# Optimization experiments

Measured on AMD Instinct MI355X. Metric: run time of the kernel, lower is better.

Reference implementation:

```python
import jax, jax.numpy as jnp
import numpy as np
import math

N_NODES = 50000
N_EDGES = 800000
IN_DIM = 128
HID = 128
OUT_DIM = 2048
N_LABEL_EDGES = 4096
POOL_RATIO = 0.5
NUM_HEADS = 8


def seg_sum(x, idx, n):
    return jax.ops.segment_sum(x, idx, num_segments=n)


def graph_conv(x, W, b, src, dst, emask, n):
    # DGL GraphConv, norm='both': D_out^-1/2 A D_in^-1/2 (x W) + b (masked edges)
    deg_out = seg_sum(emask, src, n)
    deg_in = seg_sum(emask, dst, n)
    ns = jax.lax.rsqrt(jnp.maximum(deg_out, 1.0))
    nd = jax.lax.rsqrt(jnp.maximum(deg_in, 1.0))
    h = x @ W
    msg = (h * ns[:, None])[src] * emask[:, None]
    agg = seg_sum(msg, dst, n)
    return agg * nd[:, None] + b


def conv_pool_block(x, src, dst, emask, cW, cb, sW, sb):
    # GraphConv -> ReLU -> SAGPool(top-k by GraphConv score, tanh gate) -> avg||max readout
    n = x.shape[0]
    h = jax.nn.relu(graph_conv(x, cW, cb, src, dst, emask, n))
    score = graph_conv(h, sW, sb, src, dst, emask, n)[:, 0]
    k = int(math.ceil(POOL_RATIO * n))  # static
    _, perm = jax.lax.top_k(score, k)
    h_new = h[perm] * jnp.tanh(score[perm])[:, None]
    # remap edges to the pooled node set; drop edges touching removed nodes via mask
    newid = jnp.full((n,), -1, jnp.int32).at[perm].set(jnp.arange(k, dtype=jnp.int32))
    nsrc = newid[src]
    ndst = newid[dst]
    new_mask = emask * (nsrc >= 0).astype(emask.dtype) * (ndst >= 0).astype(emask.dtype)
    nsrc = jnp.maximum(nsrc, 0)
    ndst = jnp.maximum(ndst, 0)
    readout = jnp.concatenate([h_new.mean(0), h_new.max(0)])[None, :]  # [1, 2*HID]
    return h_new, nsrc, ndst, new_mask, readout


def gat_conv(x, fcW, al, ar, lsrc, ldst, n, slope=0.2):
    # GATConv(1 -> 1, num_heads=8): head feature dim is 1
    h = x @ fcW                      # [n, heads]
    el = h * al
    er = h * ar
    e = jax.nn.leaky_relu(el[lsrc] + er[ldst], slope)  # [E_l, heads]
    emax = jax.ops.segment_max(e, ldst, num_segments=n)
    emax = jnp.where(jnp.isfinite(emax), emax, 0.0)
    ex = jnp.exp(e - emax[ldst])
    denom = seg_sum(ex, ldst, n)
    alpha = ex / jnp.maximum(denom[ldst], 1e-9)
    out = seg_sum(alpha * h[lsrc], ldst, n)            # [n, heads]
    return out[:, :, None]                             # [n, heads, 1]


def setup_inputs() -> dict:
    key = jax.random.key(0)
    ks = jax.random.split(key, 32)

    def rn(k, shape, s=0.05):
        return jax.random.normal(k, shape, jnp.float32) * s

    inp = {}
    inp['feat'] = jax.random.normal(ks[0], (N_NODES, IN_DIM), jnp.float32)
    inp['sequence_feature'] = jax.random.normal(ks[1], (1, 1024), jnp.float32)
    inp['src'] = jax.random.randint(ks[2], (N_EDGES,), 0, N_NODES, jnp.int32)
    inp['dst'] = jax.random.randint(ks[3], (N_EDGES,), 0, N_NODES, jnp.int32)
    inp['label_src'] = jax.random.randint(ks[4], (N_LABEL_EDGES,), 0, OUT_DIM, jnp.int32)
    inp['label_dst'] = jax.random.randint(ks[5], (N_LABEL_EDGES,), 0, OUT_DIM, jnp.int32)
    i = 6
    for b in range(3):
        din = IN_DIM if b == 0 else HID
        inp['cW%d' % b] = rn(ks[i], (din, HID)); i += 1
        inp['cb%d' % b] = jnp.zeros((HID,), jnp.float32)
        inp['sW%d' % b] = rn(ks[i], (HID, 1)); i += 1
        inp['sb%d' % b] = jnp.zeros((1,), jnp.float32)
    inp['lin1W'] = rn(ks[i], (2 * HID + 1024, 2 * HID)); i += 1
    inp['lin1b'] = jnp.zeros((2 * HID,), jnp.float32)
    inp['lin2W'] = rn(ks[i], (2 * HID, HID)); i += 1
    inp['lin2b'] = jnp.zeros((HID,), jnp.float32)
    inp['lin3W'] = rn(ks[i], (HID, OUT_DIM)); i += 1
    inp['lin3b'] = jnp.zeros((OUT_DIM,), jnp.float32)
    inp['gat_fcW'] = rn(ks[i], (1, NUM_HEADS)); i += 1
    inp['gat_al'] = rn(ks[i], (NUM_HEADS,)); i += 1
    inp['gat_ar'] = rn(ks[i], (NUM_HEADS,)); i += 1
    return inp


def reference(feat, sequence_feature, src, dst, label_src, label_dst,
              cW0, cb0, sW0, sb0, cW1, cb1, sW1, sb1, cW2, cb2, sW2, sb2,
              lin1W, lin1b, lin2W, lin2b, lin3W, lin3b,
              gat_fcW, gat_al, gat_ar):
    x, s, d = feat, src, dst
    emask = jnp.ones((src.shape[0],), jnp.float32)
    final = None
    for cW, cb, sW, sb in ((cW0, cb0, sW0, sb0), (cW1, cb1, sW1, sb1), (cW2, cb2, sW2, sb2)):
        x, s, d, emask, ro = conv_pool_block(x, s, d, emask, cW, cb, sW, sb)
        final = ro if final is None else final + ro
    final = jnp.concatenate([final, sequence_feature], axis=-1)  # [1, 2*HID+1024]
    f = jax.nn.relu(final @ lin1W + lin1b)
    # dropout: eval mode -> identity
    f = jax.nn.relu(f @ lin2W + lin2b)
    f = f @ lin3W + lin3b          # [1, OUT_DIM]
    ft = f.T                       # [OUT_DIM, 1]
    gat_out = gat_conv(ft, gat_fcW, gat_al, gat_ar, label_src, label_dst, OUT_DIM)
    max_value = jnp.max(gat_out, axis=1)      # [OUT_DIM, 1]
    _ = ft - jax.nn.relu(max_value)           # computed then discarded, as in source
    return ft.T
```

## Files before the change

kernel.cpp:

```cpp
#include <hip/hip_runtime.h>
#include <hip/hip_bf16.h>
#include <cmath>

#define N0 50000
#define NEDGE 800000
#define NEG_HUGE -3.402823466e38f
#define STRIDE 128
#define HBINS 12500
#define HSLICE 16

typedef int i32x4 __attribute__((ext_vector_type(4)));
typedef __attribute__((ext_vector_type(8))) short short8v;
typedef __attribute__((ext_vector_type(4))) float f32x4;

__device__ inline float b2f(unsigned short u) { return __uint_as_float(((unsigned)u) << 16); }

__device__ inline unsigned short f2b(float f) {
    __hip_bfloat16 h = __float2bfloat16(f);
    return *(unsigned short*)&h;
}

__device__ inline unsigned fkey(float f) {
    unsigned b = __float_as_uint(f);
    if (b == 0x80000000u) b = 0u;
    return (b & 0x80000000u) ? ~b : (b | 0x80000000u);
}

__device__ inline void atomicMaxF(float* a, float v) {
    if (v >= 0.f) atomicMax((int*)a, __float_as_int(v));
    else          atomicMin((unsigned int*)a, __float_as_uint(v));
}

__global__ void k_init(float* finalv, float* f1raw, int* deg_out, int* fill,
                       int* binsA, int* binsB, float* maxbuf, int* ctrl) {
    int i = blockIdx.x * blockDim.x + threadIdx.x;
    if (i < 256) { finalv[i] = 0.f; f1raw[i] = 0.f; }
    if (i < 384) maxbuf[i] = NEG_HUGE;
    if (i < N0) { deg_out[i] = 0; fill[i] = 0; }
    if (i < 65536) { binsA[i] = 0; binsB[i] = 0; }
    if (i < 2) ctrl[8 + i] = 0;
}

__global__ __launch_bounds__(1024) void k_hist(const int* __restrict__ esrc,
                                               unsigned* __restrict__ deg_part) {
    __shared__ unsigned hist[HBINS];
    int b = blockIdx.x;
    int r = b & 3;
    int slice = b >> 2;
    for (int i = threadIdx.x; i < HBINS; i += 1024) hist[i] = 0;
    __syncthreads();
    int lo = r * HBINS;
    int base = slice * (NEDGE / HSLICE);
    for (int e = threadIdx.x * 4; e < NEDGE / HSLICE; e += 4096) {
        i32x4 a = __builtin_nontemporal_load((const i32x4*)(esrc + base + e));
        int ss[4] = {a.x, a.y, a.z, a.w};
#pragma unroll
        for (int q = 0; q < 4; ++q) {
            unsigned loc = (unsigned)(ss[q] - lo);
            if (loc < (unsigned)HBINS) atomicAdd(&hist[loc], 1u);
        }
    }
    __syncthreads();
    for (int i = threadIdx.x; i < HBINS; i += 1024)
        deg_part[(size_t)slice * N0 + lo + i] = hist[i];
}

__global__ void k_dsum(const unsigned* __restrict__ deg_part, int* deg_out) {
    int v = blockIdx.x * 256 + threadIdx.x;
    if (v >= N0) return;
    unsigned s = 0;
#pragma unroll
    for (int q = 0; q < HSLICE; ++q) s += deg_part[(size_t)q * N0 + v];
    deg_out[v] = (int)s;
}

__global__ __launch_bounds__(256) void k_build(
        const int* __restrict__ esrc, const int* __restrict__ edst,
        int* fill, int* csr_src) {
    int t = blockIdx.x * 256 + threadIdx.x;
    int e0 = t * 4;
    if (e0 >= NEDGE) return;
    i32x4 a = __builtin_nontemporal_load((const i32x4*)(esrc + e0));
    i32x4 bq = __builtin_nontemporal_load((const i32x4*)(edst + e0));
    int s[4] = {a.x, a.y, a.z, a.w};
    int d[4] = {bq.x, bq.y, bq.z, bq.w};
#pragma unroll
    for (int kq = 0; kq < 4; ++kq) {
        int pos = atomicAdd(&fill[d[kq]], 1);
        if (pos < STRIDE) csr_src[(size_t)d[kq] * STRIDE + pos] = s[kq];
    }
}

__global__ __launch_bounds__(256) void k_rmbuild(
        const int* __restrict__ esrc, const int* __restrict__ edst,
        const int2* __restrict__ ein, int use_pair,
        const int* __restrict__ ctrl, int slot,
        const int* __restrict__ newid,
        int2* __restrict__ eout, int* __restrict__ outcnt,
        int* deg_out, int* fill, int* csr_src) {
    __shared__ int wbase[4];
    __shared__ int blkbase;
    int E = (slot < 0) ? NEDGE : ctrl[slot];
    if (blockIdx.x * 256 >= E) return;
    int i = blockIdx.x * 256 + threadIdx.x;
    int lane = threadIdx.x & 63, w = threadIdx.x >> 6;
    int ns = -1, nd = -1;
    if (i < E) {
        int s, d;
        if (use_pair) { int2 pr = ein[i]; s = pr.x; d = pr.y; }
        else { s = esrc[i]; d = edst[i]; }
        ns = newid[s]; nd = newid[d];
    }
    bool keep = (ns >= 0) && (nd >= 0);
    unsigned long long m = __ballot(keep);
    int rank = __popcll(m & ((1ull << lane) - 1ull));
    if (lane == 0) wbase[w] = __popcll(m);
    __syncthreads();
    if (threadIdx.x == 0)
        blkbase = atomicAdd(outcnt, wbase[0] + wbase[1] + wbase[2] + wbase[3]);
    __syncthreads();
    int base = blkbase;
    for (int q = 0; q < w; ++q) base += wbase[q];
    if (keep) {
        eout[base + rank] = make_int2(ns, nd);
        atomicAdd(&deg_out[ns], 1);
        int pos = atomicAdd(&fill[nd], 1);
        if (pos < STRIDE) csr_src[(size_t)nd * STRIDE + pos] = ns;
    }
}

__global__ __launch_bounds__(256) void k_gemm(
        const float* __restrict__ feat, const float* __restrict__ xprev,
        const int* __restrict__ oldid, const float* __restrict__ garr,
        const int* __restrict__ deg_out,
        const float* __restrict__ W, unsigned short* __restrict__ hpre,
        int n, int nprev, int mode) {
    __shared__ short Wt[128][136];
    __shared__ short Xt[64][136];
    __shared__ int ridx_s[64];
    __shared__ float esc_s[64];
    int tid = threadIdx.x;
    int r0 = blockIdx.x * 64;
    if (tid < 64) {
        int gr = r0 + tid;
        int ridx = 0; float esc = 0.f;
        if (gr < n) {
            if (mode == 0) {
                ridx = gr;
                esc = rsqrtf(fmaxf((float)deg_out[gr], 1.f));
            } else {
                int orow = oldid[gr];
                if ((unsigned)orow < (unsigned)nprev) {
                    ridx = orow;
                    esc = rsqrtf(fmaxf((float)deg_out[gr], 1.f)) * garr[gr];
                }
            }
        }
        ridx_s[tid] = ridx;
        esc_s[tid] = esc;
    }
    __syncthreads();
    {
        int col = tid & 127;
        int kh = tid >> 7;
#pragma unroll
        for (int c8 = 0; c8 < 8; ++c8) {
            int kb = kh * 64 + c8 * 8;
            unsigned short v[8];
#pragma unroll
            for (int j = 0; j < 8; ++j)
                v[j] = f2b(W[(size_t)(kb + j) * 128 + col]);
            *(uint4*)&Wt[col][kb] = *(uint4*)v;
        }
    }
    {
        const float* xsrc = (mode == 0) ? feat : xprev;
        int rr = tid >> 2;
        int kx = (tid & 3) * 32;
        const float4* xp = (const float4*)(xsrc + (size_t)ridx_s[rr] * 128 + kx);
#pragma unroll
        for (int c4 = 0; c4 < 8; ++c4) {
            float4 v = xp[c4];
            unsigned short u[4];
            u[0] = f2b(v.x); u[1] = f2b(v.y); u[2] = f2b(v.z); u[3] = f2b(v.w);
            *(uint2*)&Xt[rr][kx + c4 * 4] = *(uint2*)u;
        }
    }
    __syncthreads();

    int lane = tid & 63, w = tid >> 6;
    int row16 = lane & 15;
    int ko = (lane >> 4) * 8;
    f32x4 acc[8];
#pragma unroll
    for (int t = 0; t < 8; ++t) acc[t] = (f32x4){0.f, 0.f, 0.f, 0.f};
#pragma unroll
    for (int kc = 0; kc < 4; ++kc) {
        int kbase = kc * 32 + ko;
        short8v a = *(short8v*)&Xt[w * 16 + row16][kbase];
#pragma unroll
        for (int t = 0; t < 8; ++t) {
            short8v b = *(short8v*)&Wt[t * 16 + row16][kbase];
            acc[t] = __builtin_amdgcn_mfma_f32_16x16x32_bf16(a, b, acc[t], 0, 0, 0);
        }
    }
    int rq = (lane >> 4) * 4;
    float esc[4];
#pragma unroll
    for (int r = 0; r < 4; ++r) esc[r] = esc_s[w * 16 + rq + r];
#pragma unroll
    for (int r = 0; r < 4; ++r) {
        int gr = r0 + w * 16 + rq + r;
        if (gr < n) {
            unsigned short* op = hpre + (size_t)gr * 128;
#pragma unroll
            for (int t = 0; t < 8; ++t)
                op[t * 16 + (lane & 15)] = f2b(acc[t][r] * esc[r]);
        }
    }
}

__global__ __launch_bounds__(256) void k_agg_conv(
        const unsigned short* __restrict__ hpre, const int* __restrict__ fill,
        const int* __restrict__ deg_out,
        const int* __restrict__ csr_src,
        const float* __restrict__ cb, const float* __restrict__ sW,
        float* __restrict__ hpost, float* __restrict__ hs, int n) {
    int wid = threadIdx.x >> 6;
    int lane = threadIdx.x & 63;
    int d = blockIdx.x * 4 + wid;
    if (d >= n) return;
    int degin = fill[d];
    int cnt = min(degin, STRIDE);
    const int* bp = csr_src + (size_t)d * STRIDE;
    int half = lane >> 5;
    int l32 = lane & 31;
    float a0 = 0.f, a1 = 0.f, a2 = 0.f, a3 = 0.f;
    int j = 0;
    for (; j + 8 <= cnt; j += 8) {
        int s0 = bp[j + half];
        int s1 = bp[j + 2 + half];
        int s2 = bp[j + 4 + half];
        int s3 = bp[j + 6 + half];
        ushort4 u0 = ((const ushort4*)(hpre + (size_t)s0 * 128))[l32];
        ushort4 u1 = ((const ushort4*)(hpre + (size_t)s1 * 128))[l32];
        ushort4 u2 = ((const ushort4*)(hpre + (size_t)s2 * 128))[l32];
        ushort4 u3 = ((const ushort4*)(hpre + (size_t)s3 * 128))[l32];
        a0 += (b2f(u0.x) + b2f(u1.x)) + (b2f(u2.x) + b2f(u3.x));
        a1 += (b2f(u0.y) + b2f(u1.y)) + (b2f(u2.y) + b2f(u3.y));
        a2 += (b2f(u0.z) + b2f(u1.z)) + (b2f(u2.z) + b2f(u3.z));
        a3 += (b2f(u0.w) + b2f(u1.w)) + (b2f(u2.w) + b2f(u3.w));
    }
    for (; j < cnt; j += 2) {
        int jj = j + half;
        if (jj < cnt) {
            int s0 = bp[jj];
            ushort4 u0 = ((const ushort4*)(hpre + (size_t)s0 * 128))[l32];
            a0 += b2f(u0.x); a1 += b2f(u0.y); a2 += b2f(u0.z); a3 += b2f(u0.w);
        }
    }
    a0 += __shfl_xor(a0, 32);
    a1 += __shfl_xor(a1, 32);
    a2 += __shfl_xor(a2, 32);
    a3 += __shfl_xor(a3, 32);
    float nd2 = rsqrtf(fmaxf((float)degin, 1.f));
    int c0 = l32 * 4;
    float h0 = fmaxf(fmaf(a0, nd2, cb[c0]), 0.f);
    float h1 = fmaxf(fmaf(a1, nd2, cb[c0 + 1]), 0.f);
    float h2 = fmaxf(fmaf(a2, nd2, cb[c0 + 2]), 0.f);
    float h3 = fmaxf(fmaf(a3, nd2, cb[c0 + 3]), 0.f);
    if (half == 0)
        ((float4*)(hpost + (size_t)d * 128))[l32] = make_float4(h0, h1, h2, h3);
    float v = h0 * sW[c0] + h1 * sW[c0 + 1] + h2 * sW[c0 + 2] + h3 * sW[c0 + 3];
#pragma unroll
    for (int off = 16; off; off >>= 1) v += __shfl_down(v, off);
    if (lane == 0) hs[d] = v * rsqrtf(fmaxf((float)deg_out[d], 1.f));
}

__global__ void k_score_hist(const float* __restrict__ hs, const int* __restrict__ fill,
                             const int* __restrict__ csr_src,
                             const float* __restrict__ sb, float* score,
                             int* binsA, int n) {
    int d = blockIdx.x * blockDim.x + threadIdx.x;
    if (d >= n) return;
    int degin = fill[d];
    int cnt = min(degin, STRIDE);
    const int* bp = csr_src + (size_t)d * STRIDE;
    float sum = 0.f;
    int j = 0;
    for (; j + 8 <= cnt; j += 8) {
        int4 s0 = *(const int4*)(bp + j);
        int4 s1 = *(const int4*)(bp + j + 4);
        sum += ((hs[s0.x] + hs[s0.y]) + (hs[s0.z] + hs[s0.w])) +
               ((hs[s1.x] + hs[s1.y]) + (hs[s1.z] + hs[s1.w]));
    }
    for (; j + 4 <= cnt; j += 4) {
        int4 ss = *(const int4*)(bp + j);
        sum += (hs[ss.x] + hs[ss.y]) + (hs[ss.z] + hs[ss.w]);
    }
    for (; j < cnt; ++j) sum += hs[bp[j]];
    float sc = rsqrtf(fmaxf((float)degin, 1.f)) * sum + sb[0];
    score[d] = sc;
    atomicAdd(&binsA[fkey(sc) >> 16], 1);
}

__global__ void k_rhist2(const float* __restrict__ score, const int* __restrict__ ctrl,
                         int n, int* binsB) {
    unsigned p16 = (unsigned)ctrl[3];
    for (int i = blockIdx.x * 256 + threadIdx.x; i < n; i += gridDim.x * 256) {
        unsigned u = fkey(score[i]);
        if ((u >> 16) == p16) atomicAdd(&binsB[u & 0xFFFFu], 1);
    }
}

__global__ void k_rpick(int stage, int k0, int* ctrl, const int* __restrict__ bins) {
    __shared__ int gs[64];
    __shared__ int arr[1024];
    __shared__ int wsum[16];
    __shared__ int sChunk, sKrem;
    int t = threadIdx.x;
    {
        int c = t >> 4, sub = t & 15;
        const int4* p4 = (const int4*)(bins + (size_t)c * 1024);
        int s = 0;
#pragma unroll
        for (int q = 0; q < 16; ++q) {
            int4 v = p4[q * 16 + sub];
            s += v.x + v.y + v.z + v.w;
        }
#pragma unroll
        for (int off = 8; off; off >>= 1) s += __shfl_down(s, off, 16);
        if (sub == 0) gs[c] = s;
    }
    __syncthreads();
    if (t == 0) {
        int kneed = (stage == 0) ? k0 : ctrl[4];
        int cum = 0, c = 63;
        for (; c >= 1; --c) { int v = gs[c]; if (cum + v >= kneed) break; cum += v; }
        sChunk = c; sKrem = kneed - cum;
    }
    __syncthreads();
    int c = sChunk;
    int v = bins[(size_t)c * 1024 + t];
    arr[t] = v;
    int lane = t & 63, w = t >> 6;
    int s = v;
#pragma unroll
    for (int off = 32; off; off >>= 1) s += __shfl_down(s, off);
    if (lane == 0) wsum[w] = s;
    __syncthreads();
    if (t == 0) {
        int kneed = sKrem;
        int cum = 0, w2 = 15;
        for (; w2 >= 1; --w2) { int vv = wsum[w2]; if (cum + vv >= kneed) break; cum += vv; }
        int j = 63;
        for (; j >= 1; --j) { int vv = arr[w2 * 64 + j]; if (cum + vv >= kneed) break; cum += vv; }
        int bin = c * 1024 + w2 * 64 + j;
        if (stage == 0) { ctrl[3] = bin; ctrl[4] = kneed - cum; }
        else {
            ctrl[0] = (int)((((unsigned)ctrl[3]) << 16) | (unsigned)bin);
            ctrl[2] = kneed - cum;
        }
    }
}

__global__ __launch_bounds__(1024) void k_cemit2(
        const float* __restrict__ score, const int* __restrict__ ctrl,
        int n, int knext, int* newid, int* oldid, float* garr,
        int* deg_out, int* fill, int* binsA, int* binsB,
        const float* __restrict__ hpost, float* finalv, float* maxbuf, float invk) {
    __shared__ int wG[16], wE[16];
    __shared__ int redCG[16], redCE[16];
    __shared__ int selIdx[1024];
    __shared__ float selG[1024];
    __shared__ int selCnt;
    __shared__ float redS[1024], redM[1024];
    int b = blockIdx.x, tid = threadIdx.x;
    int lane = tid & 63, wv = tid >> 6;
    unsigned T = (unsigned)ctrl[0];
    int needEq = ctrl[2];

    if (knext > 0) {
        int gt = b * 1024 + tid, nt = gridDim.x * 1024;
        for (int z = gt; z < 65536; z += nt) { binsA[z] = 0; binsB[z] = 0; }
        for (int z = gt; z < knext; z += nt) { deg_out[z] = 0; fill[z] = 0; }
    }

    int cg_ = 0, ce_ = 0;
    int end = b << 10;
    for (int i = tid; i < end; i += 1024) {
        unsigned u = fkey(score[i]);
        cg_ += (u > T);
        ce_ += (u == T);
    }
#pragma unroll
    for (int off = 32; off; off >>= 1) {
        cg_ += __shfl_down(cg_, off);
        ce_ += __shfl_down(ce_, off);
    }
    if (lane == 0) { redCG[wv] = cg_; redCE[wv] = ce_; }
    if (tid == 0) selCnt = 0;

    int i = (b << 10) + tid;
    bool inb = (i < n);
    float sc = inb ? score[i] : 0.f;
    unsigned u = inb ? fkey(sc) : 0u;
    bool isG = inb && (u > T);
    bool isE = inb && (u == T);
    unsigned long long mG = __ballot(isG);
    unsigned long long mE = __ballot(isE);
    if (lane == 0) { wG[wv] = __popcll(mG); wE[wv] = __popcll(mE); }
    __syncthreads();

    int sGoff = 0, sEoff = 0;
#pragma unroll
    for (int w = 0; w < 16; ++w) { sGoff += redCG[w]; sEoff += redCE[w]; }
    int gW = 0, eW = 0;
    for (int w = 0; w < wv; ++w) { gW += wG[w]; eW += wE[w]; }
    unsigned long long below = (1ull << lane) - 1ull;
    int Gb = sGoff + gW + __popcll(mG & below);
    int Eb = sEoff + eW + __popcll(mE & below);
    if (inb) {
        bool sel = isG || (isE && (Eb < needEq));
        if (sel) {
            int j = Gb + min(Eb, needEq);
            newid[i] = j;
            oldid[j] = i;
            float g = tanhf(sc);
            garr[j] = g;
            int p = atomicAdd(&selCnt, 1);
            selIdx[p] = i;
            selG[p] = g;
        } else {
            newid[i] = -1;
        }
    }
    __syncthreads();

    int m = selCnt;
    int grp = tid >> 7, c = tid & 127;
    float sum = 0.f, mx = NEG_HUGE;
    for (int r = grp; r < m; r += 8) {
        float v = hpost[(size_t)selIdx[r] * 128 + c] * selG[r];
        sum += v;
        mx = fmaxf(mx, v);
    }
    redS[tid] = sum;
    redM[tid] = mx;
    __syncthreads();
    if (tid < 128) {
        float s2 = 0.f, m2 = NEG_HUGE;
#pragma unroll
        for (int g2 = 0; g2 < 8; ++g2) {
            s2 += redS[g2 * 128 + tid];
            m2 = fmaxf(m2, redM[g2 * 128 + tid]);
        }
        atomicAdd(&finalv[tid], s2 * invk);
        atomicMaxF(&maxbuf[tid], m2);
    }
}

__global__ void k_mlp1(const float* __restrict__ finalv, const float* __restrict__ maxbuf,
                       const float* __restrict__ seq, const float* __restrict__ W1,
                       float* f1raw) {
    int o = threadIdx.x;
    int j0 = blockIdx.x * 128;
    float acc = 0.f;
    for (int jj = 0; jj < 128; ++jj) {
        int j = j0 + jj;
        float fv;
        if (j < 128) fv = finalv[j];
        else if (j < 256) fv = maxbuf[j - 128] + maxbuf[j] + maxbuf[j + 128];
        else fv = seq[j - 256];
        acc = fmaf(fv, W1[(size_t)j * 256 + o], acc);
    }
    atomicAdd(&f1raw[o], acc);
}

__global__ void k_mlp2(const float* __restrict__ f1raw, const float* __restrict__ b1,
                       const float* __restrict__ W2, const float* __restrict__ bb2,
                       float* f2v) {
    __shared__ float f1s[256];
    int t = threadIdx.x;
    f1s[t] = fmaxf(f1raw[t] + b1[t], 0.f);
    f1s[t + 128] = fmaxf(f1raw[t + 128] + b1[t + 128], 0.f);
    __syncthreads();
    float acc = 0.f;
    for (int j = 0; j < 256; ++j)
        acc = fmaf(f1s[j], W2[(size_t)j * 128 + t], acc);
    f2v[t] = fmaxf(acc + bb2[t], 0.f);
}

__global__ void k_mlp3(const float* __restrict__ f2v, const float* __restrict__ W3,
                       const float* __restrict__ b3, float* out) {
    __shared__ float f2s[128];
    int t = threadIdx.x;
    f2s[t] = f2v[t];
    __syncthreads();
    int col = blockIdx.x * 128 + t;
    float acc = 0.f;
    for (int j = 0; j < 128; ++j)
        acc = fmaf(f2s[j], W3[(size_t)j * 2048 + col], acc);
    out[col] = acc + b3[col];
}

extern "C" void kernel_launch(void* const* d_in, const int* in_sizes, int n_in,
                              void* d_out, int out_size, void* d_ws, size_t ws_size,
                              hipStream_t stream) {
    (void)in_sizes; (void)n_in; (void)out_size; (void)ws_size;
    const float* feat = (const float*)d_in[0];
    const float* seq  = (const float*)d_in[1];
    const int* src = (const int*)d_in[2];
    const int* dst = (const int*)d_in[3];
    const float *cW[3], *cb[3], *sW[3], *sb[3];
    for (int b = 0; b < 3; ++b) {
        cW[b] = (const float*)d_in[6 + 4 * b];
        cb[b] = (const float*)d_in[7 + 4 * b];
        sW[b] = (const float*)d_in[8 + 4 * b];
        sb[b] = (const float*)d_in[9 + 4 * b];
    }
    const float* lin1W = (const float*)d_in[18];
    const float* lin1b = (const float*)d_in[19];
    const float* lin2W = (const float*)d_in[20];
    const float* lin2b = (const float*)d_in[21];
    const float* lin3W = (const float*)d_in[22];
    const float* lin3b = (const float*)d_in[23];
    float* out = (float*)d_out;

    char* p = (char*)d_ws;
    size_t off = 0;
    auto alloc = [&](size_t bytes) -> void* {
        void* r = p + off;
        off = (off + bytes + 255) & ~(size_t)255;
        return r;
    };
    unsigned short* hpre = (unsigned short*)alloc((size_t)N0 * 128 * 2);
    float* hpost  = (float*)alloc((size_t)N0 * 128 * 4);
    float* hs     = (float*)alloc((size_t)N0 * 4);
    float* score  = (float*)alloc((size_t)N0 * 4);
    int* deg_out  = (int*)alloc((size_t)N0 * 4);
    int* fill     = (int*)alloc((size_t)N0 * 4);
    unsigned* deg_part = (unsigned*)alloc((size_t)HSLICE * N0 * 4);
    int2* epair1  = (int2*)alloc((size_t)NEDGE * 8);
    int* csr_src  = (int*)alloc((size_t)N0 * STRIDE * 4);
    int* newid    = (int*)alloc((size_t)N0 * 4);
    int* oldid    = (int*)alloc((size_t)25000 * 4);
    float* garr   = (float*)alloc((size_t)25000 * 4);
    float* maxbuf = (float*)alloc(3 * 128 * 4);
    float* finalv = (float*)alloc(256 * 4);
    float* f1raw  = (float*)alloc(256 * 4);
    float* f2v    = (float*)alloc(128 * 4);
    int* ctrl     = (int*)alloc(64 * 4);
    int* binsA    = (int*)alloc(65536 * 4);
    int* binsB    = (int*)alloc(65536 * 4);
    int2* epair2  = (int2*)hpre;

    const int nb[3] = {50000, 25000, 12500};
    const int kb[3] = {25000, 12500, 6250};

    k_init<<<256, 256, 0, stream>>>(finalv, f1raw, deg_out, fill, binsA, binsB,
                                    maxbuf, ctrl);

    for (int b = 0; b < 3; ++b) {
        int n = nb[b], k = kb[b];
        int B = (n + 1023) / 1024;
        if (b == 0) {
            k_hist<<<64, 1024, 0, stream>>>(src, deg_part);
            k_dsum<<<(N0 + 255) / 256, 256, 0, stream>>>(deg_part, deg_out);
            k_build<<<(NEDGE / 4 + 255) / 256, 256, 0, stream>>>(src, dst, fill, csr_src);
        } else if (b == 1) {
            k_rmbuild<<<(NEDGE + 255) / 256, 256, 0, stream>>>(
                src, dst, (const int2*)0, 0, ctrl, -1, newid, epair1, ctrl + 8,
                deg_out, fill, csr_src);
        } else {
            k_rmbuild<<<(NEDGE + 255) / 256, 256, 0, stream>>>(
                (const int*)0, (const int*)0, epair1, 1, ctrl, 8, newid, epair2, ctrl + 9,
                deg_out, fill, csr_src);
        }
        k_gemm<<<(n + 63) / 64, 256, 0, stream>>>(feat, hpost, oldid, garr, deg_out, cW[b],
                                                  hpre, n, (b > 0) ? nb[b - 1] : 1,
                                                  (b == 0) ? 0 : 1);
        k_agg_conv<<<(n + 3) / 4, 256, 0, stream>>>(hpre, fill, deg_out, csr_src, cb[b],
                                                    sW[b], hpost, hs, n);
        k_score_hist<<<(n + 255) / 256, 256, 0, stream>>>(hs, fill, csr_src, sb[b],
                                                          score, binsA, n);
        k_rpick<<<1, 1024, 0, stream>>>(0, k, ctrl, binsA);
        k_rhist2<<<128, 256, 0, stream>>>(score, ctrl, n, binsB);
        k_rpick<<<1, 1024, 0, stream>>>(1, k, ctrl, binsB);
        k_cemit2<<<B, 1024, 0, stream>>>(score, ctrl, n, (b < 2) ? kb[b] : 0,
                                         newid, oldid, garr, deg_out, fill, binsA, binsB,
                                         hpost, finalv, maxbuf + b * 128,
                                         1.0f / (float)k);
    }

    k_mlp1<<<10, 256, 0, stream>>>(finalv, maxbuf, seq, lin1W, f1raw);
    k_mlp2<<<1, 128, 0, stream>>>(f1raw, lin1b, lin2W, lin2b, f2v);
    k_mlp3<<<16, 128, 0, stream>>>(f2v, lin3W, lin3b, out);
}
```

Before: 573.2 us.

## Build first-layer CSR via sliced LDS histograms instead of global atomics

Replaces the global-atomic CSR construction for the first block with a two-pass scheme. It histograms destination degrees per edge slice in shared memory, prefix-sums per-slice offsets in k_dsum, then fills CSR slots using LDS atomics per node range. Slice and bin counts are changed to 8x6250. This targets contention on global atomics over the 50k fill counters, at the cost of an extra histogram pass and more edge reads.

```diff
diff --git a/kernel.cpp b/kernel.cpp
--- a/kernel.cpp
+++ b/kernel.cpp
@@ -6,8 +6,8 @@
 #define NEDGE 800000
 #define NEG_HUGE -3.402823466e38f
 #define STRIDE 128
-#define HBINS 12500
-#define HSLICE 16
+#define HBINS 6250
+#define HSLICE 8
 
 typedef int i32x4 __attribute__((ext_vector_type(4)));
 typedef __attribute__((ext_vector_type(8))) short short8v;
@@ -41,18 +41,18 @@
     if (i < 2) ctrl[8 + i] = 0;
 }
 
-__global__ __launch_bounds__(1024) void k_hist(const int* __restrict__ esrc,
-                                               unsigned* __restrict__ deg_part) {
+__global__ __launch_bounds__(1024) void k_hist(const int* __restrict__ earr,
+                                               unsigned* __restrict__ part) {
     __shared__ unsigned hist[HBINS];
     int b = blockIdx.x;
-    int r = b & 3;
-    int slice = b >> 2;
+    int r = b & 7;
+    int slice = b >> 3;
     for (int i = threadIdx.x; i < HBINS; i += 1024) hist[i] = 0;
     __syncthreads();
     int lo = r * HBINS;
     int base = slice * (NEDGE / HSLICE);
     for (int e = threadIdx.x * 4; e < NEDGE / HSLICE; e += 4096) {
-        i32x4 a = __builtin_nontemporal_load((const i32x4*)(esrc + base + e));
+        i32x4 a = __builtin_nontemporal_load((const i32x4*)(earr + base + e));
         int ss[4] = {a.x, a.y, a.z, a.w};
 #pragma unroll
         for (int q = 0; q < 4; ++q) {
@@ -62,32 +62,52 @@
     }
     __syncthreads();
     for (int i = threadIdx.x; i < HBINS; i += 1024)
-        deg_part[(size_t)slice * N0 + lo + i] = hist[i];
-}
-
-__global__ void k_dsum(const unsigned* __restrict__ deg_part, int* deg_out) {
+        part[(size_t)slice * N0 + lo + i] = hist[i];
+}
+
+__global__ void k_dsum(const unsigned* __restrict__ dp_s, unsigned* dp_d,
+                       int* deg_out, int* fill) {
     int v = blockIdx.x * 256 + threadIdx.x;
     if (v >= N0) return;
     unsigned s = 0;
 #pragma unroll
-    for (int q = 0; q < HSLICE; ++q) s += deg_part[(size_t)q * N0 + v];
+    for (int q = 0; q < HSLICE; ++q) s += dp_s[(size_t)q * N0 + v];
     deg_out[v] = (int)s;
-}
-
-__global__ __launch_bounds__(256) void k_build(
+    unsigned off = 0;
+#pragma unroll
+    for (int q = 0; q < HSLICE; ++q) {
+        unsigned t = dp_d[(size_t)q * N0 + v];
+        dp_d[(size_t)q * N0 + v] = off;
+        off += t;
+    }
+    fill[v] = (int)off;
+}
+
+__global__ __launch_bounds__(1024) void k_fill(
         const int* __restrict__ esrc, const int* __restrict__ edst,
-        int* fill, int* csr_src) {
-    int t = blockIdx.x * 256 + threadIdx.x;
-    int e0 = t * 4;
-    if (e0 >= NEDGE) return;
-    i32x4 a = __builtin_nontemporal_load((const i32x4*)(esrc + e0));
-    i32x4 bq = __builtin_nontemporal_load((const i32x4*)(edst + e0));
-    int s[4] = {a.x, a.y, a.z, a.w};
-    int d[4] = {bq.x, bq.y, bq.z, bq.w};
-#pragma unroll
-    for (int kq = 0; kq < 4; ++kq) {
-        int pos = atomicAdd(&fill[d[kq]], 1);
-        if (pos < STRIDE) csr_src[(size_t)d[kq] * STRIDE + pos] = s[kq];
+        const unsigned* __restrict__ foff, int* csr_src) {
+    __shared__ unsigned cur[HBINS];
+    int b = blockIdx.x;
+    int r = b & 7;
+    int slice = b >> 3;
+    int lo = r * HBINS;
+    for (int i = threadIdx.x; i < HBINS; i += 1024)
+        cur[i] = foff[(size_t)slice * N0 + lo + i];
+    __syncthreads();
+    int base = slice * (NEDGE / HSLICE);
+    for (int e = threadIdx.x * 4; e < NEDGE / HSLICE; e += 4096) {
+        i32x4 sv = __builtin_nontemporal_load((const i32x4*)(esrc + base + e));
+        i32x4 dv = __builtin_nontemporal_load((const i32x4*)(edst + base + e));
+        int ss[4] = {sv.x, sv.y, sv.z, sv.w};
+        int dd[4] = {dv.x, dv.y, dv.z, dv.w};
+#pragma unroll
+        for (int q = 0; q < 4; ++q) {
+            unsigned loc = (unsigned)(dd[q] - lo);
+            if (loc < (unsigned)HBINS) {
+                unsigned pos = atomicAdd(&cur[loc], 1u);
+                if (pos < STRIDE) csr_src[(size_t)dd[q] * STRIDE + pos] = ss[q];
+            }
+        }
     }
 }
 
@@ -540,7 +560,8 @@
     float* score  = (float*)alloc((size_t)N0 * 4);
     int* deg_out  = (int*)alloc((size_t)N0 * 4);
     int* fill     = (int*)alloc((size_t)N0 * 4);
-    unsigned* deg_part = (unsigned*)alloc((size_t)HSLICE * N0 * 4);
+    unsigned* dp_s = (unsigned*)alloc((size_t)HSLICE * N0 * 4);
+    unsigned* dp_d = (unsigned*)alloc((size_t)HSLICE * N0 * 4);
     int2* epair1  = (int2*)alloc((size_t)NEDGE * 8);
     int* csr_src  = (int*)alloc((size_t)N0 * STRIDE * 4);
     int* newid    = (int*)alloc((size_t)N0 * 4);
@@ -565,9 +586,10 @@
         int n = nb[b], k = kb[b];
         int B = (n + 1023) / 1024;
         if (b == 0) {
-            k_hist<<<64, 1024, 0, stream>>>(src, deg_part);
-            k_dsum<<<(N0 + 255) / 256, 256, 0, stream>>>(deg_part, deg_out);
-            k_build<<<(NEDGE / 4 + 255) / 256, 256, 0, stream>>>(src, dst, fill, csr_src);
+            k_hist<<<64, 1024, 0, stream>>>(src, dp_s);
+            k_hist<<<64, 1024, 0, stream>>>(dst, dp_d);
+            k_dsum<<<(N0 + 255) / 256, 256, 0, stream>>>(dp_s, dp_d, deg_out, fill);
+            k_fill<<<64, 1024, 0, stream>>>(src, dst, dp_d, csr_src);
         } else if (b == 1) {
             k_rmbuild<<<(NEDGE + 255) / 256, 256, 0, stream>>>(
                 src, dst, (const int2*)0, 0, ctrl, -1, newid, epair1, ctrl + 8,
```

New measurement: 597.2 us. 4.2% more time.
